# Optimization experiments

Hardware: AMD Instinct MI355X
Metric: run time of the kernel (lower is better)

## Reference

```python
import jax, jax.numpy as jnp
import numpy as np

DIM = 512
N_PATCH = 1024
HEADS = 8
LN_EPS = 1e-5
NORM_EPS = 1e-12


def _layernorm(x, g, b):
    mu = jnp.mean(x, axis=-1, keepdims=True)
    var = jnp.mean(jnp.square(x - mu), axis=-1, keepdims=True)
    return (x - mu) * jax.lax.rsqrt(var + LN_EPS) * g + b


def _l2norm(x):
    # matches F.normalize(dim=-1): x / max(||x||, eps)
    n = jnp.sqrt(jnp.sum(jnp.square(x), axis=-1, keepdims=True))
    return x / jnp.maximum(n, NORM_EPS)


def _gelu(x):
    return jax.nn.gelu(x, approximate=False)


def _cosine_attn_branch(x, qkv_w, qkv_b, ln_g, ln_b, proj_w, proj_b, temperature):
    B, N, D = x.shape
    H = HEADS
    hd = D // H
    qkv = _layernorm(x @ qkv_w + qkv_b, ln_g, ln_b)          # [B,N,3D]
    q, k, v = jnp.split(qkv, 3, axis=-1)
    def to_heads(t):
        return t.reshape(B, N, H, hd).transpose(0, 2, 1, 3)  # [B,H,N,hd]
    q, k, v = to_heads(q), to_heads(k), to_heads(v)
    q = _l2norm(q)
    k = _l2norm(k)
    # temperature: [H,1,1] broadcasts over [B,H,N,N]
    attn = jnp.einsum('bhnd,bhmd->bhnm', q, k) * temperature
    attn = jax.nn.softmax(attn, axis=-1)
    out = jnp.einsum('bhnm,bhmd->bhnd', attn, v)
    out = out.transpose(0, 2, 1, 3).reshape(B, N, D)
    return out @ proj_w + proj_b


def setup_inputs() -> dict:
    key = jax.random.key(0)
    ks = iter(jax.random.split(key, 40))
    D = DIM
    def rn(shape, scale=0.02):
        return (jax.random.normal(next(ks), shape, dtype=jnp.float32) * scale)
    inp = {
        'hsi_tokens': jax.random.normal(next(ks), (8, N_PATCH, D), dtype=jnp.float32),
        'lidar_tokens': jax.random.normal(next(ks), (8, N_PATCH, D), dtype=jnp.float32),
        'temperature': jnp.ones((HEADS, 1, 1), dtype=jnp.float32),
        'sq_w': rn((D, 3 * D)), 'sq_b': jnp.zeros((3 * D,), jnp.float32),
        'sq_ln_g': jnp.ones((3 * D,), jnp.float32), 'sq_ln_b': jnp.zeros((3 * D,), jnp.float32),
        'sproj_w': rn((D, D)), 'sproj_b': jnp.zeros((D,), jnp.float32),
        'pq_w': rn((D, 3 * D)), 'pq_b': jnp.zeros((3 * D,), jnp.float32),
        'pq_ln_g': jnp.ones((3 * D,), jnp.float32), 'pq_ln_b': jnp.zeros((3 * D,), jnp.float32),
        'pproj_w': rn((D, D)), 'pproj_b': jnp.zeros((D,), jnp.float32),
        'vf_w1': rn((D, 2 * D)), 'vf_b1': jnp.zeros((2 * D,), jnp.float32),
        'vf_w2': rn((2 * D, D)), 'vf_b2': jnp.zeros((D,), jnp.float32),
        'ag_w1': rn((2 * D, D)), 'ag_b1': jnp.zeros((D,), jnp.float32),
        'ag_ln_g': jnp.ones((D,), jnp.float32), 'ag_ln_b': jnp.zeros((D,), jnp.float32),
        'ag_w2': rn((D, 3)), 'ag_b2': jnp.zeros((3,), jnp.float32),
        'fr_w1': rn((D, 2 * D)), 'fr_b1': jnp.zeros((2 * D,), jnp.float32),
        'fr_w2': rn((2 * D, D)), 'fr_b2': jnp.zeros((D,), jnp.float32),
        'alpha': jnp.ones((1,), jnp.float32),
        'beta': jnp.ones((1,), jnp.float32),
    }
    return inp


def reference(hsi_tokens, lidar_tokens, temperature,
              sq_w, sq_b, sq_ln_g, sq_ln_b, sproj_w, sproj_b,
              pq_w, pq_b, pq_ln_g, pq_ln_b, pproj_w, pproj_b,
              vf_w1, vf_b1, vf_w2, vf_b2,
              ag_w1, ag_b1, ag_ln_g, ag_ln_b, ag_w2, ag_b2,
              fr_w1, fr_b1, fr_w2, fr_b2, alpha, beta):
    B, N, D = hsi_tokens.shape
    out_spectral = _cosine_attn_branch(hsi_tokens, sq_w, sq_b, sq_ln_g, sq_ln_b,
                                       sproj_w, sproj_b, temperature)
    out_spatial = _cosine_attn_branch(lidar_tokens, pq_w, pq_b, pq_ln_g, pq_ln_b,
                                      pproj_w, pproj_b, temperature)
    # volumetric fusion MLP (dropout is identity in eval)
    s = out_spectral + out_spatial
    volumetric_feat = _gelu(s @ vf_w1 + vf_b1) @ vf_w2 + vf_b2
    # adaptive gating
    hsi_global = jnp.mean(out_spectral, axis=1)    # [B,D]
    lidar_global = jnp.mean(out_spatial, axis=1)   # [B,D]
    concat = jnp.concatenate([hsi_global, lidar_global], axis=-1)  # [B,2D]
    g = _gelu(_layernorm(concat @ ag_w1 + ag_b1, ag_ln_g, ag_ln_b))
    gate = jax.nn.softmax(g @ ag_w2 + ag_b2, axis=-1)  # [B,3]
    w_spec = gate[:, 0][:, None, None]
    w_spat = gate[:, 1][:, None, None]
    w_vol = gate[:, 2][:, None, None]
    fused = w_spec * out_spectral + w_spat * out_spatial + w_vol * volumetric_feat
    fused_recal = _gelu(fused @ fr_w1 + fr_b1) @ fr_w2 + fr_b2
    return fused + alpha * fused_recal + beta * (hsi_tokens + lidar_tokens) * 0.5
```

## Files before the change

### kernel.cpp

```cpp
#include <hip/hip_runtime.h>
#include <hip/hip_bf16.h>
#include <math.h>

#define B_   8
#define N_   1024
#define D_   512
#define H_   8
#define HD_  64
#define D3_  1536
#define M_   (B_ * N_)

#define WOFF_SQ    0
#define WOFF_PQ    786432
#define WOFF_SPROJ 1572864
#define WOFF_PPROJ 1835008
#define WOFF_VF1   2097152
#define WOFF_VF2   2621440
#define WOFF_FR1   3145728
#define WOFF_FR2   3670016

typedef float f32x4 __attribute__((ext_vector_type(4)));
typedef __bf16 bf16x8 __attribute__((ext_vector_type(8)));

union FragU {
    uint4 u4;
    unsigned int u[4];
    ushort s[8];
    bf16x8 v;
};

static __device__ __forceinline__ ushort f2bf(float x) {
    union { __bf16 h; ushort u; } c;
    c.h = (__bf16)x;
    return c.u;
}

static __device__ __forceinline__ float bf2f(ushort u) {
    union { unsigned u; float f; } c;
    c.u = ((unsigned)u) << 16;
    return c.f;
}

static __device__ __forceinline__ unsigned int pack2(float a, float b) {
    return (unsigned int)f2bf(a) | ((unsigned int)f2bf(b) << 16);
}

static __device__ __forceinline__ float gelu_f(float x) {
    return 0.5f * x * (1.0f + erff(x * 0.7071067811865475f));
}

#if __has_builtin(__builtin_amdgcn_exp2f)
static __device__ __forceinline__ float exp2_fast(float x) { return __builtin_amdgcn_exp2f(x); }
#else
static __device__ __forceinline__ float exp2_fast(float x) { return exp2f(x); }
#endif

static __device__ __forceinline__ void gload16(const ushort* g, ushort* lds) {
    __builtin_amdgcn_global_load_lds(
        (const __attribute__((address_space(1))) void*)g,
        (__attribute__((address_space(3))) void*)lds, 16, 0, 0);
}

static __device__ __forceinline__ float blk_sum(float v, float* red) {
    #pragma unroll
    for (int off = 32; off; off >>= 1) v += __shfl_xor(v, off);
    const int w = threadIdx.x >> 6;
    __syncthreads();
    if ((threadIdx.x & 63) == 0) red[w] = v;
    __syncthreads();
    return red[0] + red[1] + red[2] + red[3];
}

template <int BM, int BN, int ACT, int OUT, bool FINAL, bool GROUP>
__global__ __launch_bounds__(256) void pgemm_k(
    const ushort* __restrict__ A, const ushort* __restrict__ Wt,
    const ushort* __restrict__ Wt2, const float* __restrict__ bias,
    const float* __restrict__ bias2, int Msplit,
    void* __restrict__ Cv, int nbx, int Nn, int K,
    const ushort* __restrict__ fusedb, const ushort* __restrict__ resb,
    const float* __restrict__ alphap, const float* __restrict__ betap)
{
    constexpr int MI = BM / 32;
    constexpr int NJ = BN / 32;
    constexpr int CA = BM / 16;
    constexpr int CB = BN / 16;
    __shared__ ushort Asm[2][BM * 32];
    __shared__ ushort Bsm[2][BN * 32];
    const int tid = threadIdx.x;
    const int w = tid >> 6, l = tid & 63;
    const int cpx = gridDim.x >> 3;
    const int wg = (blockIdx.x & 7) * cpx + (blockIdx.x >> 3);
    const int m0 = (wg / nbx) * BM, n0 = (wg % nbx) * BN;
    const int wr = w >> 1, wc = w & 1;
    const int lr = l & 15, g = l >> 4;

    const ushort* W_ = (!GROUP || m0 < Msplit) ? Wt : Wt2;
    const float* b_ = (!GROUP || m0 < Msplit) ? bias : bias2;

    f32x4 acc[MI][NJ] = {};
    const int nt = K >> 5;

    #define STAGE(buf, kt)                                                        \
        do {                                                                      \
            const int k0s = (kt) << 5;                                            \
            for (int c = w; c < CA; c += 4)                                       \
                gload16(&A[(size_t)(m0 + c * 16 + lr) * K + k0s + 8 * g],         \
                        &Asm[buf][c * 512]);                                      \
            for (int c = w; c < CB; c += 4)                                       \
                gload16(&W_[(size_t)(n0 + c * 16 + lr) * K + k0s + 8 * g],        \
                        &Bsm[buf][c * 512]);                                      \
        } while (0)

    STAGE(0, 0);
    __syncthreads();
    int cur = 0;
    for (int t = 0; t < nt; ++t) {
        if (t + 1 < nt) STAGE(cur ^ 1, t + 1);
        FragU af[MI], bf4[NJ];
        #pragma unroll
        for (int mi = 0; mi < MI; ++mi)
            af[mi].u4 = *reinterpret_cast<const uint4*>(
                &Asm[cur][(wr * MI + mi) * 512 + l * 8]);
        #pragma unroll
        for (int nj = 0; nj < NJ; ++nj)
            bf4[nj].u4 = *reinterpret_cast<const uint4*>(
                &Bsm[cur][(wc * NJ + nj) * 512 + l * 8]);
        #pragma unroll
        for (int mi = 0; mi < MI; ++mi)
            #pragma unroll
            for (int nj = 0; nj < NJ; ++nj)
                acc[mi][nj] = __builtin_amdgcn_mfma_f32_16x16x32_bf16(
                    af[mi].v, bf4[nj].v, acc[mi][nj], 0, 0, 0);
        __syncthreads();
        cur ^= 1;
    }
    #undef STAGE

    float alpha = 0.f, beta = 0.f;
    if (FINAL) { alpha = alphap[0]; beta = betap[0]; }
    #pragma unroll
    for (int mi = 0; mi < MI; ++mi) {
        #pragma unroll
        for (int r = 0; r < 4; ++r) {
            const int m = m0 + wr * (MI * 16) + mi * 16 + g * 4 + r;
            #pragma unroll
            for (int nj = 0; nj < NJ; ++nj) {
                const int n = n0 + wc * (NJ * 16) + nj * 16 + lr;
                const size_t idx = (size_t)m * Nn + n;
                float v = acc[mi][nj][r] + b_[n];
                if (ACT == 1) v = gelu_f(v);
                if (FINAL)
                    v = bf2f(fusedb[idx]) + alpha * v + beta * bf2f(resb[idx]);
                if (OUT == 0) ((float*)Cv)[idx] = v;
                else          ((ushort*)Cv)[idx] = f2bf(v);
            }
        }
    }
}

__global__ __launch_bounds__(256) void cvtw_k(
    const float* __restrict__ w0, const float* __restrict__ w1,
    const float* __restrict__ w2, const float* __restrict__ w3,
    const float* __restrict__ w4, const float* __restrict__ w5,
    const float* __restrict__ w6, const float* __restrict__ w7,
    ushort* __restrict__ dst)
{
    __shared__ ushort T[64][72];
    const int id = blockIdx.z;
    int K, Nn, off;
    const float* src;
    switch (id) {
        case 0: src = w0; K = 512;  Nn = 1536; off = WOFF_SQ;    break;
        case 1: src = w1; K = 512;  Nn = 1536; off = WOFF_PQ;    break;
        case 2: src = w2; K = 512;  Nn = 512;  off = WOFF_SPROJ; break;
        case 3: src = w3; K = 512;  Nn = 512;  off = WOFF_PPROJ; break;
        case 4: src = w4; K = 512;  Nn = 1024; off = WOFF_VF1;   break;
        case 5: src = w5; K = 1024; Nn = 512;  off = WOFF_VF2;   break;
        case 6: src = w6; K = 512;  Nn = 1024; off = WOFF_FR1;   break;
        default: src = w7; K = 1024; Nn = 512; off = WOFF_FR2;   break;
    }
    const int n0 = blockIdx.x * 64, k0 = blockIdx.y * 64;
    if (n0 >= Nn || k0 >= K) return;
    const int t = threadIdx.x;
    const int q = t >> 6, e = t & 63;
    #pragma unroll 4
    for (int i = 0; i < 16; ++i) {
        const int kl = q * 16 + i;
        T[e][kl] = f2bf(src[(size_t)(k0 + kl) * Nn + n0 + e]);
    }
    __syncthreads();
    #pragma unroll 4
    for (int i = 0; i < 16; ++i) {
        const int nl = q * 16 + i;
        dst[(size_t)off + (size_t)(n0 + nl) * K + k0 + e] = T[nl][e];
    }
}

__global__ __launch_bounds__(256) void cvt3_k(const float* __restrict__ h,
                                              const float* __restrict__ l,
                                              ushort* __restrict__ xh,
                                              ushort* __restrict__ xl,
                                              ushort* __restrict__ rb)
{
    const size_t i = ((size_t)blockIdx.x * 256 + threadIdx.x) * 8;
    const float4 h0 = *reinterpret_cast<const float4*>(h + i);
    const float4 h1 = *reinterpret_cast<const float4*>(h + i + 4);
    const float4 l0 = *reinterpret_cast<const float4*>(l + i);
    const float4 l1 = *reinterpret_cast<const float4*>(l + i + 4);
    FragU oh, ol, orr;
    oh.u[0] = pack2(h0.x, h0.y); oh.u[1] = pack2(h0.z, h0.w);
    oh.u[2] = pack2(h1.x, h1.y); oh.u[3] = pack2(h1.z, h1.w);
    ol.u[0] = pack2(l0.x, l0.y); ol.u[1] = pack2(l0.z, l0.w);
    ol.u[2] = pack2(l1.x, l1.y); ol.u[3] = pack2(l1.z, l1.w);
    orr.u[0] = pack2(0.5f * (h0.x + l0.x), 0.5f * (h0.y + l0.y));
    orr.u[1] = pack2(0.5f * (h0.z + l0.z), 0.5f * (h0.w + l0.w));
    orr.u[2] = pack2(0.5f * (h1.x + l1.x), 0.5f * (h1.y + l1.y));
    orr.u[3] = pack2(0.5f * (h1.z + l1.z), 0.5f * (h1.w + l1.w));
    *reinterpret_cast<uint4*>(xh + i) = oh.u4;
    *reinterpret_cast<uint4*>(xl + i) = ol.u4;
    *reinterpret_cast<uint4*>(rb + i) = orr.u4;
}

__global__ __launch_bounds__(256) void cvtadd_k(const ushort* __restrict__ a,
                                                const ushort* __restrict__ b,
                                                ushort* __restrict__ dst)
{
    const size_t i = ((size_t)blockIdx.x * 256 + threadIdx.x) * 8;
    FragU x, y, o;
    x.u4 = *reinterpret_cast<const uint4*>(a + i);
    y.u4 = *reinterpret_cast<const uint4*>(b + i);
    #pragma unroll
    for (int e = 0; e < 8; ++e) o.s[e] = f2bf(bf2f(x.s[e]) + bf2f(y.s[e]));
    *reinterpret_cast<uint4*>(dst + i) = o.u4;
}

__global__ __launch_bounds__(256) void lnprep_k(ushort* __restrict__ x,
                                                const float* __restrict__ lng0,
                                                const float* __restrict__ lnb0,
                                                const float* __restrict__ lng1,
                                                const float* __restrict__ lnb1,
                                                const float* __restrict__ temp,
                                                ushort* __restrict__ Kb,
                                                ushort* __restrict__ Vt)
{
    __shared__ ushort Vs[8 * 512];
    const int w = threadIdx.x >> 6, l = threadIdx.x & 63;
    const int n0 = blockIdx.x * 8;
    const float L2E = 1.4426950408889634f;
    const float* lng = (n0 < 8192) ? lng0 : lng1;
    const float* lnb = (n0 < 8192) ? lnb0 : lnb1;

    #pragma unroll
    for (int rr = 0; rr < 2; ++rr) {
        const int row = n0 + w * 2 + rr;
        const int bb = row >> 10;
        const int n = row & 1023;
        ushort* xr = x + (size_t)row * D3_;
        float qv[24];
        #pragma unroll
        for (int i = 0; i < 24; ++i) qv[i] = bf2f(xr[l + 64 * i]);
        float s = 0.f, ss = 0.f;
        #pragma unroll
        for (int i = 0; i < 24; ++i) { s += qv[i]; ss += qv[i] * qv[i]; }
        #pragma unroll
        for (int off = 32; off; off >>= 1) {
            s += __shfl_xor(s, off);
            ss += __shfl_xor(ss, off);
        }
        const float mu = s * (1.0f / D3_);
        const float var = ss * (1.0f / D3_) - mu * mu;
        const float rs = rsqrtf(var + 1e-5f);
        #pragma unroll
        for (int i = 0; i < 24; ++i)
            qv[i] = (qv[i] - mu) * rs * lng[l + 64 * i] + lnb[l + 64 * i];
        float sq[16];
        #pragma unroll
        for (int i = 0; i < 16; ++i) sq[i] = qv[i] * qv[i];
        #pragma unroll
        for (int off = 32; off; off >>= 1)
            #pragma unroll
            for (int i = 0; i < 16; ++i) sq[i] += __shfl_xor(sq[i], off);
        #pragma unroll
        for (int i = 0; i < 8; ++i) {
            const float qs = temp[i] * L2E / fmaxf(sqrtf(sq[i]), 1e-12f);
            xr[i * 64 + l] = f2bf(qv[i] * qs);
        }
        #pragma unroll
        for (int i = 0; i < 8; ++i) {
            const float ks = 1.0f / fmaxf(sqrtf(sq[8 + i]), 1e-12f);
            Kb[((size_t)(bb * 8 + i) * N_ + n) * HD_ + l] = f2bf(qv[8 + i] * ks);
        }
        #pragma unroll
        for (int i = 0; i < 8; ++i)
            Vs[(w * 2 + rr) * 512 + i * 64 + l] = f2bf(qv[16 + i]);
    }
    __syncthreads();
    const int bb = n0 >> 10;
    #pragma unroll
    for (int it = 0; it < 2; ++it) {
        const int combo = threadIdx.x + it * 256;
        FragU f;
        #pragma unroll
        for (int tok = 0; tok < 8; ++tok) f.s[tok] = Vs[tok * 512 + combo];
        *reinterpret_cast<uint4*>(
            &Vt[((size_t)(bb * 8 + (combo >> 6)) * HD_ + (combo & 63)) * N_ + (n0 & 1023)]) = f.u4;
    }
}

__global__ __launch_bounds__(256) void fattn_k(const ushort* __restrict__ Qu,
                                               const ushort* __restrict__ Kb,
                                               const ushort* __restrict__ Vt,
                                               const float* __restrict__ temp,
                                               ushort* __restrict__ out)
{
    __shared__ ushort Ks[64 * 72];
    __shared__ ushort Vs[64 * 72];
    const int tid = threadIdx.x;
    const int cpx = gridDim.x >> 3;
    const int wg = (blockIdx.x & 7) * cpx + (blockIdx.x >> 3);
    const int nb = wg & 7;
    const int h  = (wg >> 3) & 7;
    const int bb = wg >> 6;
    const int bh = bb * 8 + h;
    const int n0 = nb * 128;
    const int w  = tid >> 6;
    const int l  = tid & 63;
    const int lr = l & 15;
    const int g  = l >> 4;
    const float m2 = fabsf(temp[h]) * 1.4426950408889634f;
    const f32x4 mInit = {-m2, -m2, -m2, -m2};

    FragU ones;
    ones.u[0] = ones.u[1] = ones.u[2] = ones.u[3] = 0x3F803F80u;

    const int qb = n0 + w * 32;
    FragU qa0, qa1, qb0, qb1;
    {
        const size_t rb0 = (size_t)(bb * N_ + qb + lr) * D3_ + h * 64 + 8 * g;
        const size_t rb1 = (size_t)(bb * N_ + qb + 16 + lr) * D3_ + h * 64 + 8 * g;
        qa0.u4 = *reinterpret_cast<const uint4*>(&Qu[rb0]);
        qa1.u4 = *reinterpret_cast<const uint4*>(&Qu[rb0 + 32]);
        qb0.u4 = *reinterpret_cast<const uint4*>(&Qu[rb1]);
        qb1.u4 = *reinterpret_cast<const uint4*>(&Qu[rb1 + 32]);
    }

    f32x4 OA[4] = {};
    f32x4 OB[4] = {};
    f32x4 LSA = {0.f, 0.f, 0.f, 0.f};
    f32x4 LSB = {0.f, 0.f, 0.f, 0.f};

    const ushort* kbase = Kb + (size_t)bh * N_ * HD_;
    const ushort* vbase = Vt + (size_t)bh * HD_ * N_;
    const int sr = tid >> 3;
    const int sc = (tid & 7) * 8;
    const int scv = sc ^ (8 * (sr & 1));
    uint4 k0r, k1r, v0r, v1r;

    #define LOADT(kt)                                                           \
        do {                                                                    \
            const ushort* ks_ = kbase + (size_t)((kt) * 64) * HD_;              \
            const ushort* vs_ = vbase + (kt) * 64;                              \
            k0r = *reinterpret_cast<const uint4*>(ks_ + sr * HD_ + sc);         \
            k1r = *reinterpret_cast<const uint4*>(ks_ + (sr + 32) * HD_ + sc);  \
            v0r = *reinterpret_cast<const uint4*>(vs_ + (size_t)sr * N_ + sc);  \
            v1r = *reinterpret_cast<const uint4*>(vs_ + (size_t)(sr + 32) * N_ + sc); \
        } while (0)
    #define WRITET()                                                            \
        do {                                                                    \
            *reinterpret_cast<uint4*>(&Ks[sr * 72 + sc]) = k0r;                 \
            *reinterpret_cast<uint4*>(&Ks[(sr + 32) * 72 + sc]) = k1r;          \
            *reinterpret_cast<uint4*>(&Vs[sr * 72 + scv]) = v0r;                \
            *reinterpret_cast<uint4*>(&Vs[(sr + 32) * 72 + scv]) = v1r;         \
        } while (0)

    LOADT(0);
    WRITET();
    __syncthreads();

    #pragma unroll 1
    for (int kt = 0; kt < 16; ++kt) {
        if (kt < 15) LOADT(kt + 1);

        unsigned paA[2][4], paB[2][4];
        #pragma unroll
        for (int j = 0; j < 4; ++j) {
            FragU ka, kc;
            ka.u4 = *reinterpret_cast<const uint4*>(&Ks[(j * 16 + lr) * 72 + 8 * g]);
            kc.u4 = *reinterpret_cast<const uint4*>(&Ks[(j * 16 + lr) * 72 + 32 + 8 * g]);
            f32x4 sA = mInit, sB = mInit;
            sA = __builtin_amdgcn_mfma_f32_16x16x32_bf16(ka.v, qa0.v, sA, 0, 0, 0);
            sA = __builtin_amdgcn_mfma_f32_16x16x32_bf16(kc.v, qa1.v, sA, 0, 0, 0);
            sB = __builtin_amdgcn_mfma_f32_16x16x32_bf16(ka.v, qb0.v, sB, 0, 0, 0);
            sB = __builtin_amdgcn_mfma_f32_16x16x32_bf16(kc.v, qb1.v, sB, 0, 0, 0);
            float pA[4], pB[4];
            #pragma unroll
            for (int r = 0; r < 4; ++r) {
                pA[r] = exp2_fast(sA[r]);
                pB[r] = exp2_fast(sB[r]);
            }
            paA[j >> 1][2 * (j & 1) + 0] = pack2(pA[0], pA[1]);
            paA[j >> 1][2 * (j & 1) + 1] = pack2(pA[2], pA[3]);
            paB[j >> 1][2 * (j & 1) + 0] = pack2(pB[0], pB[1]);
            paB[j >> 1][2 * (j & 1) + 1] = pack2(pB[2], pB[3]);
        }

        #pragma unroll
        for (int ks = 0; ks < 2; ++ks) {
            FragU fa, fb2;
            fa.u[0] = paA[ks][0]; fa.u[1] = paA[ks][1];
            fa.u[2] = paA[ks][2]; fa.u[3] = paA[ks][3];
            fb2.u[0] = paB[ks][0]; fb2.u[1] = paB[ks][1];
            fb2.u[2] = paB[ks][2]; fb2.u[3] = paB[ks][3];
            LSA = __builtin_amdgcn_mfma_f32_16x16x32_bf16(fa.v, ones.v, LSA, 0, 0, 0);
            LSB = __builtin_amdgcn_mfma_f32_16x16x32_bf16(fb2.v, ones.v, LSB, 0, 0, 0);
            #pragma unroll
            for (int s4 = 0; s4 < 4; ++s4) {
                FragU vb;
                const int vi = (lr + 16 * s4) * 72 + ((ks * 32 + 4 * g) ^ (8 * (lr & 1)));
                *reinterpret_cast<uint2*>(&vb.u[0]) =
                    *reinterpret_cast<const uint2*>(&Vs[vi]);
                *reinterpret_cast<uint2*>(&vb.u[2]) =
                    *reinterpret_cast<const uint2*>(&Vs[vi + 16]);
                OA[s4] = __builtin_amdgcn_mfma_f32_16x16x32_bf16(fa.v, vb.v, OA[s4], 0, 0, 0);
                OB[s4] = __builtin_amdgcn_mfma_f32_16x16x32_bf16(fb2.v, vb.v, OB[s4], 0, 0, 0);
            }
        }

        if (kt < 15) {
            __syncthreads();
            WRITET();
            __syncthreads();
        }
    }
    #undef LOADT
    #undef WRITET

    ushort* outp = out + ((size_t)(bb * N_) + qb) * D_ + h * HD_;
    #pragma unroll
    for (int r = 0; r < 4; ++r) {
        const float iA = 1.0f / LSA[r];
        const float iB = 1.0f / LSB[r];
        ushort* rowA = outp + (size_t)(4 * g + r) * D_;
        ushort* rowB = outp + (size_t)(16 + 4 * g + r) * D_;
        #pragma unroll
        for (int s4 = 0; s4 < 4; ++s4) {
            rowA[s4 * 16 + lr] = f2bf(OA[s4][r] * iA);
            rowB[s4 * 16 + lr] = f2bf(OB[s4][r] * iB);
        }
    }
}

__global__ __launch_bounds__(256) void means_k(const ushort* __restrict__ spec,
                                               const ushort* __restrict__ spat,
                                               float* __restrict__ Gp)
{
    const int b = blockIdx.x >> 5;
    const int ch = blockIdx.x & 31;
    const int n0 = ch * 32;
    const int d0 = threadIdx.x * 2;
    float s1a = 0.f, s1b = 0.f, s2a = 0.f, s2b = 0.f;
    #pragma unroll 4
    for (int n = 0; n < 32; ++n) {
        const size_t idx = ((size_t)(b * N_) + n0 + n) * D_ + d0;
        ushort u1[2], u2[2];
        *reinterpret_cast<unsigned*>(u1) = *reinterpret_cast<const unsigned*>(spec + idx);
        *reinterpret_cast<unsigned*>(u2) = *reinterpret_cast<const unsigned*>(spat + idx);
        s1a += bf2f(u1[0]); s1b += bf2f(u1[1]);
        s2a += bf2f(u2[0]); s2b += bf2f(u2[1]);
    }
    float* gp = Gp + (size_t)blockIdx.x * 1024;
    gp[d0] = s1a; gp[d0 + 1] = s1b;
    gp[512 + d0] = s2a; gp[512 + d0 + 1] = s2b;
}

__global__ __launch_bounds__(256) void gate1_k(const float* __restrict__ Gp,
                                               const float* __restrict__ w1,
                                               const float* __restrict__ b1,
                                               float* __restrict__ y)
{
    __shared__ float xs[1024];
    __shared__ float red[4][64];
    const int jc = blockIdx.x, b = blockIdx.y, tid = threadIdx.x;
    for (int k = tid; k < 1024; k += 256) {
        float s = 0.f;
        #pragma unroll 8
        for (int c = 0; c < 32; ++c) s += Gp[(size_t)(b * 32 + c) * 1024 + k];
        xs[k] = s * (1.0f / N_);
    }
    __syncthreads();
    const int jl = tid & 63;
    const int jj = jc * 64 + jl;
    const int seg = tid >> 6;
    float acc = 0.f;
    const float* wp = w1 + (size_t)(seg * 256) * 512 + jj;
    const float* xp = xs + seg * 256;
    #pragma unroll 8
    for (int k = 0; k < 256; ++k) acc += xp[k] * wp[(size_t)k * 512];
    red[seg][jl] = acc;
    __syncthreads();
    if (tid < 64)
        y[b * 512 + jc * 64 + tid] =
            red[0][tid] + red[1][tid] + red[2][tid] + red[3][tid] + b1[jc * 64 + tid];
}

__global__ __launch_bounds__(256) void gate2_k(const float* __restrict__ y,
                                               const float* __restrict__ lng,
                                               const float* __restrict__ lnb,
                                               const float* __restrict__ w2,
                                               const float* __restrict__ b2,
                                               float* __restrict__ gate)
{
    __shared__ float red[4];
    const int b = blockIdx.x, tid = threadIdx.x;
    const float v0 = y[b * 512 + tid];
    const float v1 = y[b * 512 + 256 + tid];
    const float s = blk_sum(v0 + v1, red);
    const float ss = blk_sum(v0 * v0 + v1 * v1, red);
    const float mu = s * (1.0f / 512.0f);
    const float var = ss * (1.0f / 512.0f) - mu * mu;
    const float rs = rsqrtf(var + 1e-5f);
    const float z0 = gelu_f((v0 - mu) * rs * lng[tid] + lnb[tid]);
    const float z1 = gelu_f((v1 - mu) * rs * lng[tid + 256] + lnb[tid + 256]);
    float p0 = z0 * w2[tid * 3 + 0] + z1 * w2[(tid + 256) * 3 + 0];
    float p1 = z0 * w2[tid * 3 + 1] + z1 * w2[(tid + 256) * 3 + 1];
    float p2 = z0 * w2[tid * 3 + 2] + z1 * w2[(tid + 256) * 3 + 2];
    p0 = blk_sum(p0, red);
    p1 = blk_sum(p1, red);
    p2 = blk_sum(p2, red);
    if (tid == 0) {
        p0 += b2[0]; p1 += b2[1]; p2 += b2[2];
        const float m = fmaxf(p0, fmaxf(p1, p2));
        const float e0 = expf(p0 - m), e1 = expf(p1 - m), e2 = expf(p2 - m);
        const float inv = 1.0f / (e0 + e1 + e2);
        gate[b * 3 + 0] = e0 * inv;
        gate[b * 3 + 1] = e1 * inv;
        gate[b * 3 + 2] = e2 * inv;
    }
}

__global__ __launch_bounds__(256) void fuse_k(
    const ushort* __restrict__ spec, const ushort* __restrict__ spat,
    const ushort* __restrict__ volb, const float* __restrict__ gate,
    ushort* __restrict__ fb)
{
    const size_t i4 = ((size_t)blockIdx.x * 256 + threadIdx.x) * 4;
    const int b = (int)(i4 >> 19);
    const float g0 = gate[b * 3 + 0], g1 = gate[b * 3 + 1], g2 = gate[b * 3 + 2];
    ushort au[4], cu[4], vu[4];
    *reinterpret_cast<uint2*>(au) = *reinterpret_cast<const uint2*>(spec + i4);
    *reinterpret_cast<uint2*>(cu) = *reinterpret_cast<const uint2*>(spat + i4);
    *reinterpret_cast<uint2*>(vu) = *reinterpret_cast<const uint2*>(volb + i4);
    union { ushort s[4]; uint2 u; } ob;
    #pragma unroll
    for (int e = 0; e < 4; ++e)
        ob.s[e] = f2bf(g0 * bf2f(au[e]) + g1 * bf2f(cu[e]) + g2 * bf2f(vu[e]));
    *reinterpret_cast<uint2*>(fb + i4) = ob.u;
}

extern "C" void kernel_launch(void* const* d_in, const int* in_sizes, int n_in,
                              void* d_out, int out_size, void* d_ws, size_t ws_size,
                              hipStream_t stream)
{
    const float* hsi    = (const float*)d_in[0];
    const float* lidar  = (const float*)d_in[1];
    const float* temp   = (const float*)d_in[2];
    const float* sq_w   = (const float*)d_in[3];
    const float* sq_b   = (const float*)d_in[4];
    const float* sq_lng = (const float*)d_in[5];
    const float* sq_lnb = (const float*)d_in[6];
    const float* sproj_w = (const float*)d_in[7];
    const float* sproj_b = (const float*)d_in[8];
    const float* pq_w   = (const float*)d_in[9];
    const float* pq_b   = (const float*)d_in[10];
    const float* pq_lng = (const float*)d_in[11];
    const float* pq_lnb = (const float*)d_in[12];
    const float* pproj_w = (const float*)d_in[13];
    const float* pproj_b = (const float*)d_in[14];
    const float* vf_w1  = (const float*)d_in[15];
    const float* vf_b1  = (const float*)d_in[16];
    const float* vf_w2  = (const float*)d_in[17];
    const float* vf_b2  = (const float*)d_in[18];
    const float* ag_w1  = (const float*)d_in[19];
    const float* ag_b1  = (const float*)d_in[20];
    const float* ag_lng = (const float*)d_in[21];
    const float* ag_lnb = (const float*)d_in[22];
    const float* ag_w2  = (const float*)d_in[23];
    const float* ag_b2  = (const float*)d_in[24];
    const float* fr_w1  = (const float*)d_in[25];
    const float* fr_b1  = (const float*)d_in[26];
    const float* fr_w2  = (const float*)d_in[27];
    const float* fr_b2  = (const float*)d_in[28];
    const float* alpha  = (const float*)d_in[29];
    const float* beta   = (const float*)d_in[30];
    float* out = (float*)d_out;

    ushort* base = (ushort*)d_ws;
    ushort* Qkv  = base;
    ushort* Ob   = base;
    ushort* Sb   = base + 8388608;
    ushort* volb = base + 12582912;
    ushort* fb   = base + 16777216;
    float*  Gp   = (float*)(base + 20971520);
    float*  gate = Gp + 262144;
    float*  ybuf = gate + 64;
    ushort* Kb   = base + 25165824;
    ushort* Vt   = base + 33554432;
    ushort* Hb   = base + 25165824;
    ushort* Ab   = base + 41943040;
    ushort* Xb   = base + 41943040;
    ushort* Wb   = base + 50331648;
    ushort* Rb   = base + 54525952;

    const dim3 blk(256);

    cvtw_k<<<dim3(24, 16, 8), blk, 0, stream>>>(sq_w, pq_w, sproj_w, pproj_w,
                                                vf_w1, vf_w2, fr_w1, fr_w2, Wb);
    cvt3_k<<<2048, blk, 0, stream>>>(hsi, lidar, Xb, Xb + (size_t)M_ * D_, Rb);

    pgemm_k<128,128,0,1,false,true><<<1536, blk, 0, stream>>>(
        Xb, Wb + WOFF_SQ, Wb + WOFF_PQ, sq_b, pq_b, M_,
        Qkv, 12, D3_, D_, nullptr, nullptr, nullptr, nullptr);

    lnprep_k<<<2048, blk, 0, stream>>>(Qkv, sq_lng, sq_lnb, pq_lng, pq_lnb,
                                       temp, Kb, Vt);

    fattn_k<<<1024, blk, 0, stream>>>(Qkv, Kb, Vt, temp, Ab);

    pgemm_k<128,64,0,1,false,true><<<1024, blk, 0, stream>>>(
        Ab, Wb + WOFF_SPROJ, Wb + WOFF_PPROJ, sproj_b, pproj_b, M_,
        Ob, 8, D_, D_, nullptr, nullptr, nullptr, nullptr);

    const ushort* spec_b = Ob;
    const ushort* spat_b = Ob + (size_t)M_ * D_;

    means_k<<<256, blk, 0, stream>>>(spec_b, spat_b, Gp);
    gate1_k<<<dim3(8, 8), blk, 0, stream>>>(Gp, ag_w1, ag_b1, ybuf);
    gate2_k<<<B_, blk, 0, stream>>>(ybuf, ag_lng, ag_lnb, ag_w2, ag_b2, gate);

    cvtadd_k<<<2048, blk, 0, stream>>>(spec_b, spat_b, Sb);
    pgemm_k<128,64,1,1,false,false><<<1024, blk, 0, stream>>>(
        Sb, Wb + WOFF_VF1, nullptr, vf_b1, nullptr, 0,
        Hb, 16, 1024, D_, nullptr, nullptr, nullptr, nullptr);
    pgemm_k<128,64,0,1,false,false><<<512, blk, 0, stream>>>(
        Hb, Wb + WOFF_VF2, nullptr, vf_b2, nullptr, 0,
        volb, 8, D_, 1024, nullptr, nullptr, nullptr, nullptr);

    fuse_k<<<4096, blk, 0, stream>>>(spec_b, spat_b, volb, gate, fb);
    pgemm_k<128,64,1,1,false,false><<<1024, blk, 0, stream>>>(
        fb, Wb + WOFF_FR1, nullptr, fr_b1, nullptr, 0,
        Hb, 16, 1024, D_, nullptr, nullptr, nullptr, nullptr);
    pgemm_k<128,64,0,0,true,false><<<512, blk, 0, stream>>>(
        Hb, Wb + WOFF_FR2, nullptr, fr_b2, nullptr, 0,
        out, 8, D_, 1024, fb, Rb, alpha, beta);
}
```

Before: 355.3 us.

## Double-buffer K/V shared tiles in flash attention with one barrier per tile

```diff
diff --git a/kernel.cpp b/kernel.cpp
--- a/kernel.cpp
+++ b/kernel.cpp
@@ -313,8 +313,8 @@
                                                const float* __restrict__ temp,
                                                ushort* __restrict__ out)
 {
-    __shared__ ushort Ks[64 * 72];
-    __shared__ ushort Vs[64 * 72];
+    __shared__ ushort Ks[2][64 * 72];
+    __shared__ ushort Vs[2][64 * 72];
     const int tid = threadIdx.x;
     const int cpx = gridDim.x >> 3;
     const int wg = (blockIdx.x & 7) * cpx + (blockIdx.x >> 3);
@@ -353,7 +353,6 @@
     const ushort* vbase = Vt + (size_t)bh * HD_ * N_;
     const int sr = tid >> 3;
     const int sc = (tid & 7) * 8;
-    const int scv = sc ^ (8 * (sr & 1));
     uint4 k0r, k1r, v0r, v1r;
 
     #define LOADT(kt)                                                           \
@@ -365,28 +364,29 @@
             v0r = *reinterpret_cast<const uint4*>(vs_ + (size_t)sr * N_ + sc);  \
             v1r = *reinterpret_cast<const uint4*>(vs_ + (size_t)(sr + 32) * N_ + sc); \
         } while (0)
-    #define WRITET()                                                            \
+    #define WRITET(p)                                                           \
         do {                                                                    \
-            *reinterpret_cast<uint4*>(&Ks[sr * 72 + sc]) = k0r;                 \
-            *reinterpret_cast<uint4*>(&Ks[(sr + 32) * 72 + sc]) = k1r;          \
-            *reinterpret_cast<uint4*>(&Vs[sr * 72 + scv]) = v0r;                \
-            *reinterpret_cast<uint4*>(&Vs[(sr + 32) * 72 + scv]) = v1r;         \
+            *reinterpret_cast<uint4*>(&Ks[p][sr * 72 + sc]) = k0r;              \
+            *reinterpret_cast<uint4*>(&Ks[p][(sr + 32) * 72 + sc]) = k1r;       \
+            *reinterpret_cast<uint4*>(&Vs[p][sr * 72 + sc]) = v0r;              \
+            *reinterpret_cast<uint4*>(&Vs[p][(sr + 32) * 72 + sc]) = v1r;       \
         } while (0)
 
     LOADT(0);
-    WRITET();
-    __syncthreads();
+    WRITET(0);
 
     #pragma unroll 1
     for (int kt = 0; kt < 16; ++kt) {
+        const int p = kt & 1;
+        __syncthreads();
         if (kt < 15) LOADT(kt + 1);
 
         unsigned paA[2][4], paB[2][4];
         #pragma unroll
         for (int j = 0; j < 4; ++j) {
             FragU ka, kc;
-            ka.u4 = *reinterpret_cast<const uint4*>(&Ks[(j * 16 + lr) * 72 + 8 * g]);
-            kc.u4 = *reinterpret_cast<const uint4*>(&Ks[(j * 16 + lr) * 72 + 32 + 8 * g]);
+            ka.u4 = *reinterpret_cast<const uint4*>(&Ks[p][(j * 16 + lr) * 72 + 8 * g]);
+            kc.u4 = *reinterpret_cast<const uint4*>(&Ks[p][(j * 16 + lr) * 72 + 32 + 8 * g]);
             f32x4 sA = mInit, sB = mInit;
             sA = __builtin_amdgcn_mfma_f32_16x16x32_bf16(ka.v, qa0.v, sA, 0, 0, 0);
             sA = __builtin_amdgcn_mfma_f32_16x16x32_bf16(kc.v, qa1.v, sA, 0, 0, 0);
@@ -404,6 +404,7 @@
             paB[j >> 1][2 * (j & 1) + 1] = pack2(pB[2], pB[3]);
         }
 
+        __builtin_amdgcn_s_setprio(1);
         #pragma unroll
         for (int ks = 0; ks < 2; ++ks) {
             FragU fa, fb2;
@@ -416,21 +417,18 @@
             #pragma unroll
             for (int s4 = 0; s4 < 4; ++s4) {
                 FragU vb;
-                const int vi = (lr + 16 * s4) * 72 + ((ks * 32 + 4 * g) ^ (8 * (lr & 1)));
+                const int vi = (lr + 16 * s4) * 72 + ks * 32 + 4 * g;
                 *reinterpret_cast<uint2*>(&vb.u[0]) =
-                    *reinterpret_cast<const uint2*>(&Vs[vi]);
+                    *reinterpret_cast<const uint2*>(&Vs[p][vi]);
                 *reinterpret_cast<uint2*>(&vb.u[2]) =
-                    *reinterpret_cast<const uint2*>(&Vs[vi + 16]);
+                    *reinterpret_cast<const uint2*>(&Vs[p][vi + 16]);
                 OA[s4] = __builtin_amdgcn_mfma_f32_16x16x32_bf16(fa.v, vb.v, OA[s4], 0, 0, 0);
                 OB[s4] = __builtin_amdgcn_mfma_f32_16x16x32_bf16(fb2.v, vb.v, OB[s4], 0, 0, 0);
             }
         }
-
-        if (kt < 15) {
-            __syncthreads();
-            WRITET();
-            __syncthreads();
-        }
+        __builtin_amdgcn_s_setprio(0);
+
+        if (kt < 15) WRITET(p ^ 1);
     }
     #undef LOADT
     #undef WRITET
```

New measurement: 350.2 us. About the same (-1.4%).
